# Kernel optimization log

Measured on AMD Instinct MI355X. Metric: run time of the kernel, lower is better.

The kernel has to match this reference:

```python
import jax, jax.numpy as jnp
import numpy as np

N, E, IN, HID, HEADS, OUT = 50000, 800000, 128, 64, 4, 64


def setup_inputs() -> dict:
    key = jax.random.key(0)
    ks = jax.random.split(key, 13)
    s1 = 1.0 / np.sqrt(IN)
    s2 = 1.0 / np.sqrt(HID * HEADS)
    s3 = 1.0 / np.sqrt(HID)
    return {
        'x': jax.random.normal(ks[0], (N, IN), dtype=jnp.float32),
        'edge_index': jax.random.randint(ks[1], (2, E), 0, N, dtype=jnp.int64),
        # GATv2 layer 1: heads=HEADS, out=HID, concat=True
        'W1l': jax.random.normal(ks[2], (IN, HEADS * HID), dtype=jnp.float32) * s1,
        'W1r': jax.random.normal(ks[3], (IN, HEADS * HID), dtype=jnp.float32) * s1,
        'att1': jax.random.normal(ks[4], (HEADS, HID), dtype=jnp.float32) * s3,
        'b1': jnp.zeros((HEADS * HID,), dtype=jnp.float32),
        # GATv2 layer 2: heads=1, out=HID
        'W2l': jax.random.normal(ks[5], (HEADS * HID, HID), dtype=jnp.float32) * s2,
        'W2r': jax.random.normal(ks[6], (HEADS * HID, HID), dtype=jnp.float32) * s2,
        'att2': jax.random.normal(ks[7], (1, HID), dtype=jnp.float32) * s3,
        'b2': jnp.zeros((HID,), dtype=jnp.float32),
        # final Linear(HID, OUT)
        'Wlin': jax.random.normal(ks[8], (HID, OUT), dtype=jnp.float32) * s3,
        'blin': jnp.zeros((OUT,), dtype=jnp.float32),
    }


def _gatv2(x, src, dst, Wl, Wr, att, bias, n):
    # PyG GATv2Conv (share_weights=False): x_j -> lin_l, x_i -> lin_r
    H, C = att.shape
    xl = (x @ Wl).reshape(n, H, C)  # source transform [N,H,C]
    xr = (x @ Wr).reshape(n, H, C)  # destination transform [N,H,C]
    # per-edge GATv2 score: a^T LeakyReLU(xl_j + xr_i)
    e = jnp.sum(jax.nn.leaky_relu(xl[src] + xr[dst], 0.2) * att, axis=-1)  # [E,H]
    # scatter-softmax over edges sharing a destination
    m = jax.ops.segment_max(e, dst, num_segments=n)  # [N,H]
    ex = jnp.exp(e - m[dst])
    denom = jax.ops.segment_sum(ex, dst, num_segments=n)
    alpha = ex / (denom[dst] + 1e-16)  # [E,H]
    # weighted scatter-add aggregation of source features
    out = jax.ops.segment_sum(xl[src] * alpha[:, :, None], dst, num_segments=n)  # [N,H,C]
    return out.reshape(n, H * C) + bias


def reference(x, edge_index, W1l, W1r, att1, b1, W2l, W2r, att2, b2, Wlin, blin):
    n = x.shape[0]
    loops = jnp.arange(n, dtype=edge_index.dtype)
    src = jnp.concatenate([edge_index[0], loops])  # add_self_loops=True (PyG default)
    dst = jnp.concatenate([edge_index[1], loops])
    h = _gatv2(x, src, dst, W1l, W1r, att1, b1, n)
    h = jax.nn.elu(h)
    h = _gatv2(h, src, dst, W2l, W2r, att2, b2, n)
    h = jax.nn.elu(h)
    return h @ Wlin + blin
```

## Files before the change

### kernel.cpp

```cpp
#include <hip/hip_runtime.h>
#include <hip/hip_bf16.h>
#include <math.h>

#define N_NODES 50000
#define N_EDGES 800000
#define ETOT (N_EDGES + N_NODES)
#define NB_SCAN 196

typedef __attribute__((ext_vector_type(8))) short short8;
typedef __attribute__((ext_vector_type(4))) float floatx4;
typedef __attribute__((ext_vector_type(2))) float f32x2;

__device__ __forceinline__ float bf_lo(unsigned u) { return __uint_as_float(u << 16); }
__device__ __forceinline__ float bf_hi(unsigned u) { return __uint_as_float(u & 0xffff0000u); }
__device__ __forceinline__ unsigned short f2bf(float f) {
    unsigned u = __float_as_uint(f);
    return (unsigned short)((u + 0x7fffu + ((u >> 16) & 1u)) >> 16);
}
__device__ __forceinline__ unsigned pack2bf(float a, float b) {
    return (unsigned)f2bf(a) | ((unsigned)f2bf(b) << 16);
}
#define DPP_ADD(p, ctrl) \
    (p) += __int_as_float(__builtin_amdgcn_update_dpp(0, __float_as_int(p), (ctrl), 0xF, 0xF, true))

__global__ __launch_bounds__(256) void k_prep(const float* __restrict__ W1l,
                                              const float* __restrict__ W1r,
                                              const float* __restrict__ W2l,
                                              const float* __restrict__ W2r,
                                              const float* __restrict__ Wlin,
                                              unsigned short* __restrict__ Wt1,
                                              unsigned short* __restrict__ Wt2,
                                              unsigned short* __restrict__ Wt3,
                                              int* __restrict__ deg) {
    const int b = blockIdx.x;
    if (b < 400) {
        const int idx = b * 256 + threadIdx.x;
        if (idx < 65536) {
            const int k = idx >> 9;
            const int n = idx & 511;
            const float v = (n < 256) ? W1l[k * 256 + n] : W1r[k * 256 + (n - 256)];
            Wt1[n * 128 + k] = f2bf(v);
        } else if (idx < 98304) {
            const int j = idx - 65536;
            const int k = j >> 7;
            const int n = j & 127;
            const float v = (n < 64) ? W2l[k * 64 + n] : W2r[k * 64 + (n - 64)];
            Wt2[n * 256 + k] = f2bf(v);
        } else {
            const int j = idx - 98304;
            const int n = j >> 6, k = j & 63;
            Wt3[n * 64 + k] = f2bf(Wlin[k * 64 + n]);
        }
    } else {
        const int i = (b - 400) * 256 + threadIdx.x;
        if (i < N_NODES) deg[i] = 0;
    }
}

__global__ __launch_bounds__(256) void k_g1h(const float* __restrict__ x,
                                             const unsigned short* __restrict__ Wt1,
                                             unsigned short* __restrict__ xlb,
                                             unsigned short* __restrict__ xrb,
                                             const int* __restrict__ ei,
                                             int* __restrict__ deg) {
    __shared__ unsigned short sA[128 * 136];
    const int b = blockIdx.x;
    if (b >= 782) {
        for (long e = (long)(b - 782) * 256 + threadIdx.x; e < ETOT; e += 1024 * 256) {
            const int d = (e < N_EDGES) ? ei[N_EDGES + e] : (int)(e - N_EDGES);
            atomicAdd(&deg[d], 1);
        }
        return;
    }
    const int t = threadIdx.x;
    const int lane = t & 63, wv = t >> 6;
    const int m0 = (b >> 1) * 128;
    const int flavor = b & 1;
#pragma unroll
    for (int j = 0; j < 16; j++) {
        const int i4 = t + j * 256;
        const int row = i4 >> 5, k4 = i4 & 31;
        float4 v = make_float4(0.f, 0.f, 0.f, 0.f);
        if (m0 + row < N_NODES) v = ((const float4*)x)[(long)(m0 + row) * 32 + k4];
        ushort4 u;
        u.x = f2bf(v.x); u.y = f2bf(v.y); u.z = f2bf(v.z); u.w = f2bf(v.w);
        *(ushort4*)&sA[row * 136 + k4 * 4] = u;
    }
    __syncthreads();
    const int l15 = lane & 15, quad = lane >> 4;
    const int nloc0 = wv * 64;
    unsigned short* outp = flavor ? xrb : xlb;
    short8 bfr[4][4];
#pragma unroll
    for (int nt = 0; nt < 4; nt++)
#pragma unroll
        for (int ks = 0; ks < 4; ks++)
            bfr[nt][ks] = *(const short8*)&Wt1[(flavor * 256 + nloc0 + nt * 16 + l15) * 128 + ks * 32 + quad * 8];
    for (int mt = 0; mt < 8; mt++) {
        short8 a[4];
#pragma unroll
        for (int ks = 0; ks < 4; ks++)
            a[ks] = *(const short8*)&sA[(mt * 16 + l15) * 136 + ks * 32 + quad * 8];
        floatx4 acc[4];
#pragma unroll
        for (int nt = 0; nt < 4; nt++) {
            acc[nt] = (floatx4)(0.f);
#pragma unroll
            for (int ks = 0; ks < 4; ks++)
                acc[nt] = __builtin_amdgcn_mfma_f32_16x16x32_bf16(a[ks], bfr[nt][ks], acc[nt], 0, 0, 0);
        }
        const int mrow0 = m0 + mt * 16 + quad * 4;
#pragma unroll
        for (int nt = 0; nt < 4; nt++) {
            const int n = nloc0 + nt * 16 + l15;
#pragma unroll
            for (int r = 0; r < 4; r++) {
                const int m = mrow0 + r;
                if (m < N_NODES) outp[(long)m * 256 + n] = f2bf(acc[nt][r]);
            }
        }
    }
}

__global__ __launch_bounds__(256) void k_scan1(const int* __restrict__ deg,
                                               int* __restrict__ rowstart,
                                               int* __restrict__ blocksum) {
    __shared__ int wsum[4];
    const int t = threadIdx.x, lane = t & 63, wv = t >> 6;
    const int i = blockIdx.x * 256 + t;
    const int v = (i < N_NODES) ? deg[i] : 0;
    int incl = v;
#pragma unroll
    for (int off = 1; off < 64; off <<= 1) {
        const int u = __shfl_up(incl, off);
        if (lane >= off) incl += u;
    }
    if (lane == 63) wsum[wv] = incl;
    __syncthreads();
    int woff = 0;
#pragma unroll
    for (int j = 0; j < 4; j++) woff += (j < wv) ? wsum[j] : 0;
    const int excl = incl - v + woff;
    if (i < N_NODES) rowstart[i] = excl;
    if (t == 255) blocksum[blockIdx.x] = excl + v;
}

__global__ __launch_bounds__(256) void k_scan2(const int* __restrict__ blocksum,
                                               int* __restrict__ blockoff) {
    __shared__ int wsum[4];
    const int t = threadIdx.x, lane = t & 63, wv = t >> 6;
    const int v = (t < NB_SCAN) ? blocksum[t] : 0;
    int incl = v;
#pragma unroll
    for (int off = 1; off < 64; off <<= 1) {
        const int u = __shfl_up(incl, off);
        if (lane >= off) incl += u;
    }
    if (lane == 63) wsum[wv] = incl;
    __syncthreads();
    int woff = 0;
#pragma unroll
    for (int j = 0; j < 4; j++) woff += (j < wv) ? wsum[j] : 0;
    if (t < NB_SCAN) blockoff[t] = incl - v + woff;
}

__global__ __launch_bounds__(256) void k_scan3(int* __restrict__ rowstart,
                                               const int* __restrict__ blockoff,
                                               int* __restrict__ cursor) {
    const int i = blockIdx.x * 256 + threadIdx.x;
    if (i < N_NODES) {
        const int r = rowstart[i] + blockoff[blockIdx.x];
        rowstart[i] = r;
        cursor[i] = r;
    }
}

__global__ __launch_bounds__(256) void k_scatter(const int* __restrict__ ei,
                                                 int* __restrict__ cursor,
                                                 int* __restrict__ csr) {
    const long e = (long)blockIdx.x * 256 + threadIdx.x;
    if (e >= ETOT) return;
    int s, d;
    if (e < N_EDGES) { s = ei[e]; d = ei[N_EDGES + e]; }
    else { s = d = (int)(e - N_EDGES); }
    const int pos = atomicAdd(&cursor[d], 1);
    csr[pos] = s << 9;
}

__global__ __launch_bounds__(256) void k_node1(const int* __restrict__ rowstart,
                                               const int* __restrict__ deg,
                                               const int* __restrict__ csr,
                                               const uint4* __restrict__ xlb,
                                               const uint4* __restrict__ xrb,
                                               const float* __restrict__ att,
                                               const float* __restrict__ b1,
                                               uint4* __restrict__ h1b) {
    const int lane = threadIdx.x & 63;
    const int wv = threadIdx.x >> 6;
    const int node = blockIdx.x * 4 + wv;
    const int g = lane >> 5;
    const int l = lane & 31;
    const char* xlbase = (const char*)xlb;
    const uint4 xru = xrb[(long)node * 32 + l];
    const float4 ta = ((const float4*)att)[2 * l];
    const float4 tb = ((const float4*)att)[2 * l + 1];
    f32x2 xp[4], tp[4];
    xp[0] = (f32x2){bf_lo(xru.x), bf_hi(xru.x)};
    xp[1] = (f32x2){bf_lo(xru.y), bf_hi(xru.y)};
    xp[2] = (f32x2){bf_lo(xru.z), bf_hi(xru.z)};
    xp[3] = (f32x2){bf_lo(xru.w), bf_hi(xru.w)};
    tp[0] = (f32x2){ta.x, ta.y}; tp[1] = (f32x2){ta.z, ta.w};
    tp[2] = (f32x2){tb.x, tb.y}; tp[3] = (f32x2){tb.z, tb.w};
    const int start = rowstart[node];
    const int cnt = deg[node];
    const int ns = (cnt - g + 1) >> 1;
    float den = 0.f;
    f32x2 acc[4];
#pragma unroll
    for (int c = 0; c < 4; c++) acc[c] = (f32x2)(0.f);

    auto body = [&](const uint4& rr) {
        f32x2 a0, a1, a2, a3;
        a0.x = bf_lo(rr.x); a0.y = bf_hi(rr.x);
        a1.x = bf_lo(rr.y); a1.y = bf_hi(rr.y);
        a2.x = bf_lo(rr.z); a2.y = bf_hi(rr.z);
        a3.x = bf_lo(rr.w); a3.y = bf_hi(rr.w);
        f32x2 v = a0 + xp[0];
        f32x2 p2 = __builtin_elementwise_max(v, v * 0.2f) * tp[0];
        v = a1 + xp[1]; p2 += __builtin_elementwise_max(v, v * 0.2f) * tp[1];
        v = a2 + xp[2]; p2 += __builtin_elementwise_max(v, v * 0.2f) * tp[2];
        v = a3 + xp[3]; p2 += __builtin_elementwise_max(v, v * 0.2f) * tp[3];
        float p = p2.x + p2.y;
        DPP_ADD(p, 0xB1);
        DPP_ADD(p, 0x4E);
        DPP_ADD(p, 0x141);
        const float w = __expf(p);
        acc[0] += a0 * w;
        acc[1] += a1 * w;
        acc[2] += a2 * w;
        acc[3] += a3 * w;
        den += w;
    };

    uint4 rcur = make_uint4(0, 0, 0, 0), rnext = rcur;
    if (ns > 0) rcur = *((const uint4*)(xlbase + csr[start + g]) + l);
    if (ns > 1) rnext = *((const uint4*)(xlbase + csr[start + 2 + g]) + l);
    int i = 0;
    for (; i + 2 < ns; i++) {
        const uint4 r2 = *((const uint4*)(xlbase + csr[start + 2 * (i + 2) + g]) + l);
        body(rcur);
        rcur = rnext; rnext = r2;
    }
    for (; i < ns; i++) {
        body(rcur);
        rcur = rnext;
    }
    den += __shfl_xor(den, 32);
    const float inv = 1.f / (den + 1e-16f);
#pragma unroll
    for (int c = 0; c < 4; c++) {
        f32x2 t2 = acc[c];
        t2.x += __shfl_xor(t2.x, 32);
        t2.y += __shfl_xor(t2.y, 32);
        acc[c] = t2;
    }
    const float4 ba = ((const float4*)b1)[2 * l];
    const float4 bb = ((const float4*)b1)[2 * l + 1];
    f32x2 bp[4];
    bp[0] = (f32x2){ba.x, ba.y}; bp[1] = (f32x2){ba.z, ba.w};
    bp[2] = (f32x2){bb.x, bb.y}; bp[3] = (f32x2){bb.z, bb.w};
    float o[8];
#pragma unroll
    for (int c = 0; c < 4; c++) {
        f32x2 t2 = acc[c] * inv + bp[c];
        o[2 * c]     = t2.x > 0.f ? t2.x : expm1f(t2.x);
        o[2 * c + 1] = t2.y > 0.f ? t2.y : expm1f(t2.y);
    }
    if (g == 0) {
        uint4 u;
        u.x = pack2bf(o[0], o[1]);
        u.y = pack2bf(o[2], o[3]);
        u.z = pack2bf(o[4], o[5]);
        u.w = pack2bf(o[6], o[7]);
        h1b[(long)node * 32 + l] = u;
    }
}

__global__ __launch_bounds__(256) void k_gemm2(const uint4* __restrict__ h,
                                               const unsigned short* __restrict__ Wt2,
                                               unsigned short* __restrict__ xlb,
                                               unsigned short* __restrict__ xrb) {
    __shared__ unsigned short sA[64 * 264];
    const int t = threadIdx.x;
    const int lane = t & 63, wv = t >> 6;
    const int m0 = blockIdx.x * 64;
#pragma unroll
    for (int j = 0; j < 8; j++) {
        const int i8 = t + j * 256;
        const int row = i8 >> 5, c8 = i8 & 31;
        uint4 v = make_uint4(0, 0, 0, 0);
        if (m0 + row < N_NODES) v = h[(long)(m0 + row) * 32 + c8];
        *(uint4*)&sA[row * 264 + c8 * 8] = v;
    }
    __syncthreads();
    const int l15 = lane & 15, quad = lane >> 4;
    const int ncol0 = wv * 32;
    short8 b[2][8];
#pragma unroll
    for (int nt = 0; nt < 2; nt++)
#pragma unroll
        for (int ks = 0; ks < 8; ks++)
            b[nt][ks] = *(const short8*)&Wt2[(ncol0 + nt * 16 + l15) * 256 + ks * 32 + quad * 8];
    for (int mt = 0; mt < 4; mt++) {
        floatx4 acc[2];
        acc[0] = (floatx4)(0.f);
        acc[1] = (floatx4)(0.f);
#pragma unroll
        for (int ks = 0; ks < 8; ks++) {
            const short8 a = *(const short8*)&sA[(mt * 16 + l15) * 264 + ks * 32 + quad * 8];
            acc[0] = __builtin_amdgcn_mfma_f32_16x16x32_bf16(a, b[0][ks], acc[0], 0, 0, 0);
            acc[1] = __builtin_amdgcn_mfma_f32_16x16x32_bf16(a, b[1][ks], acc[1], 0, 0, 0);
        }
        const int mrow0 = m0 + mt * 16 + quad * 4;
#pragma unroll
        for (int nt = 0; nt < 2; nt++) {
            const int n = ncol0 + nt * 16 + l15;
#pragma unroll
            for (int r = 0; r < 4; r++) {
                const int m = mrow0 + r;
                if (m < N_NODES) {
                    if (n < 64) xlb[(long)m * 64 + n] = f2bf(acc[nt][r]);
                    else        xrb[(long)m * 64 + (n - 64)] = f2bf(acc[nt][r]);
                }
            }
        }
    }
}

__global__ __launch_bounds__(256) void k_node2(const int* __restrict__ rowstart,
                                               const int* __restrict__ deg,
                                               const int* __restrict__ csr,
                                               const uint2* __restrict__ xlb,
                                               const uint2* __restrict__ xrb,
                                               const float* __restrict__ att,
                                               const float* __restrict__ b2,
                                               uint2* __restrict__ h2b) {
    const int lane = threadIdx.x & 63;
    const int wv = threadIdx.x >> 6;
    const int node = blockIdx.x * 4 + wv;
    const int g = lane >> 4;
    const int l = lane & 15;
    const char* xlbase = (const char*)xlb;
    const uint2 xru = xrb[(long)node * 16 + l];
    const float4 at4 = ((const float4*)att)[l];
    f32x2 xp[2], tp[2];
    xp[0] = (f32x2){bf_lo(xru.x), bf_hi(xru.x)};
    xp[1] = (f32x2){bf_lo(xru.y), bf_hi(xru.y)};
    tp[0] = (f32x2){at4.x, at4.y}; tp[1] = (f32x2){at4.z, at4.w};
    const int start = rowstart[node];
    const int cnt = deg[node];
    const int ns = (cnt - g + 3) >> 2;
    float den = 0.f;
    f32x2 acc[2];
    acc[0] = (f32x2)(0.f); acc[1] = (f32x2)(0.f);

    auto body = [&](const uint2& rr) {
        f32x2 a0, a1;
        a0.x = bf_lo(rr.x); a0.y = bf_hi(rr.x);
        a1.x = bf_lo(rr.y); a1.y = bf_hi(rr.y);
        f32x2 v = a0 + xp[0];
        f32x2 p2 = __builtin_elementwise_max(v, v * 0.2f) * tp[0];
        v = a1 + xp[1]; p2 += __builtin_elementwise_max(v, v * 0.2f) * tp[1];
        float p = p2.x + p2.y;
        DPP_ADD(p, 0xB1);
        DPP_ADD(p, 0x4E);
        DPP_ADD(p, 0x141);
        DPP_ADD(p, 0x140);
        const float w = __expf(p);
        acc[0] += a0 * w;
        acc[1] += a1 * w;
        den += w;
    };

    uint2 rcur = make_uint2(0, 0), rnext = rcur;
    if (ns > 0) rcur = *((const uint2*)(xlbase + (csr[start + g] >> 2)) + l);
    if (ns > 1) rnext = *((const uint2*)(xlbase + (csr[start + 4 + g] >> 2)) + l);
    int i = 0;
    for (; i + 2 < ns; i++) {
        const uint2 r2 = *((const uint2*)(xlbase + (csr[start + 4 * (i + 2) + g] >> 2)) + l);
        body(rcur);
        rcur = rnext; rnext = r2;
    }
    for (; i < ns; i++) {
        body(rcur);
        rcur = rnext;
    }
    den += __shfl_xor(den, 16);
    den += __shfl_xor(den, 32);
    const float inv = 1.f / (den + 1e-16f);
    float t0 = acc[0].x, t1 = acc[0].y, t2 = acc[1].x, t3 = acc[1].y;
    t0 += __shfl_xor(t0, 16); t0 += __shfl_xor(t0, 32);
    t1 += __shfl_xor(t1, 16); t1 += __shfl_xor(t1, 32);
    t2 += __shfl_xor(t2, 16); t2 += __shfl_xor(t2, 32);
    t3 += __shfl_xor(t3, 16); t3 += __shfl_xor(t3, 32);
    const float4 b4 = ((const float4*)b2)[l];
    float4 h4;
    h4.x = t0 * inv + b4.x; h4.x = h4.x > 0.f ? h4.x : expm1f(h4.x);
    h4.y = t1 * inv + b4.y; h4.y = h4.y > 0.f ? h4.y : expm1f(h4.y);
    h4.z = t2 * inv + b4.z; h4.z = h4.z > 0.f ? h4.z : expm1f(h4.z);
    h4.w = t3 * inv + b4.w; h4.w = h4.w > 0.f ? h4.w : expm1f(h4.w);
    if (g == 0) {
        uint2 u;
        u.x = pack2bf(h4.x, h4.y);
        u.y = pack2bf(h4.z, h4.w);
        h2b[(long)node * 16 + l] = u;
    }
}

__global__ __launch_bounds__(256) void k_gemm3(const uint4* __restrict__ h2,
                                               const unsigned short* __restrict__ Wt3,
                                               const float* __restrict__ blin,
                                               float* __restrict__ out) {
    __shared__ unsigned short sA[64 * 72];
    const int t = threadIdx.x;
    const int lane = t & 63, wv = t >> 6;
    const int m0 = blockIdx.x * 64;
#pragma unroll
    for (int j = 0; j < 2; j++) {
        const int i8 = t + j * 256;
        const int row = i8 >> 3, c8 = i8 & 7;
        uint4 v = make_uint4(0, 0, 0, 0);
        if (m0 + row < N_NODES) v = h2[(long)(m0 + row) * 8 + c8];
        *(uint4*)&sA[row * 72 + c8 * 8] = v;
    }
    __syncthreads();
    const int l15 = lane & 15, quad = lane >> 4;
    const int n0 = wv * 16;
    const short8 b0 = *(const short8*)&Wt3[(n0 + l15) * 64 + quad * 8];
    const short8 b1 = *(const short8*)&Wt3[(n0 + l15) * 64 + 32 + quad * 8];
    const float bl = blin[n0 + l15];
#pragma unroll
    for (int mt = 0; mt < 4; mt++) {
        const short8 a0 = *(const short8*)&sA[(mt * 16 + l15) * 72 + quad * 8];
        const short8 a1 = *(const short8*)&sA[(mt * 16 + l15) * 72 + 32 + quad * 8];
        floatx4 acc = (floatx4)(0.f);
        acc = __builtin_amdgcn_mfma_f32_16x16x32_bf16(a0, b0, acc, 0, 0, 0);
        acc = __builtin_amdgcn_mfma_f32_16x16x32_bf16(a1, b1, acc, 0, 0, 0);
        const int mrow0 = m0 + mt * 16 + quad * 4;
#pragma unroll
        for (int r = 0; r < 4; r++) {
            const int m = mrow0 + r;
            if (m < N_NODES) out[(long)m * 64 + n0 + l15] = acc[r] + bl;
        }
    }
}

extern "C" void kernel_launch(void* const* d_in, const int* in_sizes, int n_in,
                              void* d_out, int out_size, void* d_ws, size_t ws_size,
                              hipStream_t stream) {
    (void)in_sizes; (void)n_in; (void)out_size; (void)ws_size;
    const float* x    = (const float*)d_in[0];
    const int*   ei   = (const int*)d_in[1];
    const float* W1l  = (const float*)d_in[2];
    const float* W1r  = (const float*)d_in[3];
    const float* att1 = (const float*)d_in[4];
    const float* b1   = (const float*)d_in[5];
    const float* W2l  = (const float*)d_in[6];
    const float* W2r  = (const float*)d_in[7];
    const float* att2 = (const float*)d_in[8];
    const float* b2   = (const float*)d_in[9];
    const float* Wlin = (const float*)d_in[10];
    const float* blin = (const float*)d_in[11];

    float* ws = (float*)d_ws;
    unsigned short* XL1b = (unsigned short*)(ws);
    uint2*          H2b  = (uint2*)(ws);
    unsigned short* XR1b = (unsigned short*)(ws + 6400000);
    uint4*          H1b  = (uint4*)(ws + 12800000);
    unsigned short* XL2b = (unsigned short*)(ws + 19200000);
    unsigned short* XR2b = (unsigned short*)(ws + 20800000);
    int* deg      = (int*)(ws + 22400000);
    int* rowstart = deg + 50000;
    int* cursor   = rowstart + 50000;
    int* blocksum = cursor + 50000;
    int* blockoff = blocksum + 256;
    int* csr      = blockoff + 256;
    unsigned short* Wt1 = (unsigned short*)(ws + 23500000);
    unsigned short* Wt2 = (unsigned short*)(ws + 23550000);
    unsigned short* Wt3 = (unsigned short*)(ws + 23600000);

    k_prep<<<596, 256, 0, stream>>>(W1l, W1r, W2l, W2r, Wlin, Wt1, Wt2, Wt3, deg);
    k_g1h<<<1806, 256, 0, stream>>>(x, Wt1, XL1b, XR1b, ei, deg);
    k_scan1<<<NB_SCAN, 256, 0, stream>>>(deg, rowstart, blocksum);
    k_scan2<<<1, 256, 0, stream>>>(blocksum, blockoff);
    k_scan3<<<NB_SCAN, 256, 0, stream>>>(rowstart, blockoff, cursor);
    k_scatter<<<(ETOT + 255) / 256, 256, 0, stream>>>(ei, cursor, csr);
    k_node1<<<12500, 256, 0, stream>>>(rowstart, deg, csr,
                                       (const uint4*)XL1b, (const uint4*)XR1b,
                                       att1, b1, H1b);
    k_gemm2<<<782, 256, 0, stream>>>((const uint4*)H1b, Wt2, XL2b, XR2b);
    k_node2<<<12500, 256, 0, stream>>>(rowstart, deg, csr,
                                       (const uint2*)XL2b, (const uint2*)XR2b,
                                       att2, b2, H2b);
    k_gemm3<<<782, 256, 0, stream>>>((const uint4*)H2b, Wt3, blin, (float*)d_out);
}
```

Measured before the change: 309.7 us.

## Merge CSR build into cooperative kernel, widen node1 lanes, use exp2 with prescaled att

Replaces the three scan kernels and the scatter kernel with one cooperative kernel that uses grid-wide syncs, removing three launch boundaries. k_node1 now processes four edges per wave concurrently, with each 16-lane group covering 16 channels (one head), instead of two edges with 32 lanes. Both node kernels switch to a native exp2 with attention vectors prescaled by log2(e) in the prep kernel. This risks cooperative launch limits and adds grid-sync overhead plus higher register pressure in node1.

```diff
diff --git a/kernel.cpp b/kernel.cpp
--- a/kernel.cpp
+++ b/kernel.cpp
@@ -1,6 +1,9 @@
 #include <hip/hip_runtime.h>
 #include <hip/hip_bf16.h>
+#include <hip/hip_cooperative_groups.h>
 #include <math.h>
+
+namespace cg = cooperative_groups;
 
 #define N_NODES 50000
 #define N_EDGES 800000
@@ -23,17 +26,23 @@
 #define DPP_ADD(p, ctrl) \
     (p) += __int_as_float(__builtin_amdgcn_update_dpp(0, __float_as_int(p), (ctrl), 0xF, 0xF, true))
 
+#define LOG2E 1.4426950408889634f
+
 __global__ __launch_bounds__(256) void k_prep(const float* __restrict__ W1l,
                                               const float* __restrict__ W1r,
                                               const float* __restrict__ W2l,
                                               const float* __restrict__ W2r,
                                               const float* __restrict__ Wlin,
+                                              const float* __restrict__ att1,
+                                              const float* __restrict__ att2,
                                               unsigned short* __restrict__ Wt1,
                                               unsigned short* __restrict__ Wt2,
                                               unsigned short* __restrict__ Wt3,
+                                              float* __restrict__ att1s,
+                                              float* __restrict__ att2s,
                                               int* __restrict__ deg) {
     const int b = blockIdx.x;
-    if (b < 400) {
+    if (b < 402) {
         const int idx = b * 256 + threadIdx.x;
         if (idx < 65536) {
             const int k = idx >> 9;
@@ -46,13 +55,19 @@
             const int n = j & 127;
             const float v = (n < 64) ? W2l[k * 64 + n] : W2r[k * 64 + (n - 64)];
             Wt2[n * 256 + k] = f2bf(v);
-        } else {
+        } else if (idx < 102400) {
             const int j = idx - 98304;
             const int n = j >> 6, k = j & 63;
             Wt3[n * 64 + k] = f2bf(Wlin[k * 64 + n]);
+        } else if (idx < 102656) {
+            const int j = idx - 102400;
+            att1s[j] = att1[j] * LOG2E;
+        } else if (idx < 102720) {
+            const int j = idx - 102656;
+            att2s[j] = att2[j] * LOG2E;
         }
     } else {
-        const int i = (b - 400) * 256 + threadIdx.x;
+        const int i = (b - 402) * 256 + threadIdx.x;
         if (i < N_NODES) deg[i] = 0;
     }
 }
@@ -122,167 +137,186 @@
     }
 }
 
-__global__ __launch_bounds__(256) void k_scan1(const int* __restrict__ deg,
-                                               int* __restrict__ rowstart,
-                                               int* __restrict__ blocksum) {
+__global__ __launch_bounds__(256) void k_csr(const int* __restrict__ deg,
+                                             int* __restrict__ rowstart,
+                                             int* __restrict__ blocksum,
+                                             int* __restrict__ blockoff,
+                                             int* __restrict__ cursor,
+                                             const int* __restrict__ ei,
+                                             int* __restrict__ csr) {
+    cg::grid_group grid = cg::this_grid();
     __shared__ int wsum[4];
     const int t = threadIdx.x, lane = t & 63, wv = t >> 6;
-    const int i = blockIdx.x * 256 + t;
-    const int v = (i < N_NODES) ? deg[i] : 0;
-    int incl = v;
-#pragma unroll
-    for (int off = 1; off < 64; off <<= 1) {
-        const int u = __shfl_up(incl, off);
-        if (lane >= off) incl += u;
-    }
-    if (lane == 63) wsum[wv] = incl;
-    __syncthreads();
-    int woff = 0;
-#pragma unroll
-    for (int j = 0; j < 4; j++) woff += (j < wv) ? wsum[j] : 0;
-    const int excl = incl - v + woff;
-    if (i < N_NODES) rowstart[i] = excl;
-    if (t == 255) blocksum[blockIdx.x] = excl + v;
-}
-
-__global__ __launch_bounds__(256) void k_scan2(const int* __restrict__ blocksum,
-                                               int* __restrict__ blockoff) {
-    __shared__ int wsum[4];
-    const int t = threadIdx.x, lane = t & 63, wv = t >> 6;
-    const int v = (t < NB_SCAN) ? blocksum[t] : 0;
-    int incl = v;
-#pragma unroll
-    for (int off = 1; off < 64; off <<= 1) {
-        const int u = __shfl_up(incl, off);
-        if (lane >= off) incl += u;
-    }
-    if (lane == 63) wsum[wv] = incl;
-    __syncthreads();
-    int woff = 0;
-#pragma unroll
-    for (int j = 0; j < 4; j++) woff += (j < wv) ? wsum[j] : 0;
-    if (t < NB_SCAN) blockoff[t] = incl - v + woff;
-}
-
-__global__ __launch_bounds__(256) void k_scan3(int* __restrict__ rowstart,
-                                               const int* __restrict__ blockoff,
-                                               int* __restrict__ cursor) {
-    const int i = blockIdx.x * 256 + threadIdx.x;
-    if (i < N_NODES) {
-        const int r = rowstart[i] + blockoff[blockIdx.x];
-        rowstart[i] = r;
-        cursor[i] = r;
-    }
-}
-
-__global__ __launch_bounds__(256) void k_scatter(const int* __restrict__ ei,
-                                                 int* __restrict__ cursor,
-                                                 int* __restrict__ csr) {
-    const long e = (long)blockIdx.x * 256 + threadIdx.x;
-    if (e >= ETOT) return;
-    int s, d;
-    if (e < N_EDGES) { s = ei[e]; d = ei[N_EDGES + e]; }
-    else { s = d = (int)(e - N_EDGES); }
-    const int pos = atomicAdd(&cursor[d], 1);
-    csr[pos] = s << 9;
-}
-
-__global__ __launch_bounds__(256) void k_node1(const int* __restrict__ rowstart,
-                                               const int* __restrict__ deg,
-                                               const int* __restrict__ csr,
-                                               const uint4* __restrict__ xlb,
-                                               const uint4* __restrict__ xrb,
-                                               const float* __restrict__ att,
-                                               const float* __restrict__ b1,
-                                               uint4* __restrict__ h1b) {
+    if (blockIdx.x < NB_SCAN) {
+        const int i = blockIdx.x * 256 + t;
+        const int v = (i < N_NODES) ? deg[i] : 0;
+        int incl = v;
+#pragma unroll
+        for (int off = 1; off < 64; off <<= 1) {
+            const int u = __shfl_up(incl, off);
+            if (lane >= off) incl += u;
+        }
+        if (lane == 63) wsum[wv] = incl;
+        __syncthreads();
+        int woff = 0;
+#pragma unroll
+        for (int j = 0; j < 4; j++) woff += (j < wv) ? wsum[j] : 0;
+        const int excl = incl - v + woff;
+        if (i < N_NODES) rowstart[i] = excl;
+        if (t == 255) blocksum[blockIdx.x] = excl + v;
+    }
+    grid.sync();
+    if (blockIdx.x == 0) {
+        const int v = (t < NB_SCAN) ? blocksum[t] : 0;
+        int incl = v;
+#pragma unroll
+        for (int off = 1; off < 64; off <<= 1) {
+            const int u = __shfl_up(incl, off);
+            if (lane >= off) incl += u;
+        }
+        __syncthreads();
+        if (lane == 63) wsum[wv] = incl;
+        __syncthreads();
+        int woff = 0;
+#pragma unroll
+        for (int j = 0; j < 4; j++) woff += (j < wv) ? wsum[j] : 0;
+        if (t < NB_SCAN) blockoff[t] = incl - v + woff;
+    }
+    grid.sync();
+    for (int c = blockIdx.x; c < NB_SCAN; c += gridDim.x) {
+        const int i = c * 256 + t;
+        if (i < N_NODES) {
+            const int r = rowstart[i] + blockoff[c];
+            rowstart[i] = r;
+            cursor[i] = r;
+        }
+    }
+    grid.sync();
+    for (long e = (long)blockIdx.x * 256 + t; e < ETOT; e += (long)gridDim.x * 256) {
+        int s, d;
+        if (e < N_EDGES) { s = ei[e]; d = ei[N_EDGES + e]; }
+        else { s = d = (int)(e - N_EDGES); }
+        const int pos = atomicAdd(&cursor[d], 1);
+        csr[pos] = s << 9;
+    }
+}
+
+__global__ __launch_bounds__(256, 4) void k_node1(const int* __restrict__ rowstart,
+                                                  const int* __restrict__ deg,
+                                                  const int* __restrict__ csr,
+                                                  const uint4* __restrict__ xlb,
+                                                  const uint4* __restrict__ xrb,
+                                                  const float* __restrict__ att_s,
+                                                  const float* __restrict__ b1,
+                                                  uint4* __restrict__ h1b) {
     const int lane = threadIdx.x & 63;
     const int wv = threadIdx.x >> 6;
     const int node = blockIdx.x * 4 + wv;
-    const int g = lane >> 5;
-    const int l = lane & 31;
+    const int g = lane >> 4;
+    const int l = lane & 15;
     const char* xlbase = (const char*)xlb;
-    const uint4 xru = xrb[(long)node * 32 + l];
-    const float4 ta = ((const float4*)att)[2 * l];
-    const float4 tb = ((const float4*)att)[2 * l + 1];
-    f32x2 xp[4], tp[4];
-    xp[0] = (f32x2){bf_lo(xru.x), bf_hi(xru.x)};
-    xp[1] = (f32x2){bf_lo(xru.y), bf_hi(xru.y)};
-    xp[2] = (f32x2){bf_lo(xru.z), bf_hi(xru.z)};
-    xp[3] = (f32x2){bf_lo(xru.w), bf_hi(xru.w)};
-    tp[0] = (f32x2){ta.x, ta.y}; tp[1] = (f32x2){ta.z, ta.w};
-    tp[2] = (f32x2){tb.x, tb.y}; tp[3] = (f32x2){tb.z, tb.w};
+    const uint4 xru0 = xrb[(long)node * 32 + 2 * l];
+    const uint4 xru1 = xrb[(long)node * 32 + 2 * l + 1];
+    f32x2 xp[8], tp[8];
+    xp[0] = (f32x2){bf_lo(xru0.x), bf_hi(xru0.x)};
+    xp[1] = (f32x2){bf_lo(xru0.y), bf_hi(xru0.y)};
+    xp[2] = (f32x2){bf_lo(xru0.z), bf_hi(xru0.z)};
+    xp[3] = (f32x2){bf_lo(xru0.w), bf_hi(xru0.w)};
+    xp[4] = (f32x2){bf_lo(xru1.x), bf_hi(xru1.x)};
+    xp[5] = (f32x2){bf_lo(xru1.y), bf_hi(xru1.y)};
+    xp[6] = (f32x2){bf_lo(xru1.z), bf_hi(xru1.z)};
+    xp[7] = (f32x2){bf_lo(xru1.w), bf_hi(xru1.w)};
+    {
+        const float4 ta0 = ((const float4*)att_s)[4 * l];
+        const float4 ta1 = ((const float4*)att_s)[4 * l + 1];
+        const float4 ta2 = ((const float4*)att_s)[4 * l + 2];
+        const float4 ta3 = ((const float4*)att_s)[4 * l + 3];
+        tp[0] = (f32x2){ta0.x, ta0.y}; tp[1] = (f32x2){ta0.z, ta0.w};
+        tp[2] = (f32x2){ta1.x, ta1.y}; tp[3] = (f32x2){ta1.z, ta1.w};
+        tp[4] = (f32x2){ta2.x, ta2.y}; tp[5] = (f32x2){ta2.z, ta2.w};
+        tp[6] = (f32x2){ta3.x, ta3.y}; tp[7] = (f32x2){ta3.z, ta3.w};
+    }
     const int start = rowstart[node];
     const int cnt = deg[node];
-    const int ns = (cnt - g + 1) >> 1;
+    const int ns = (cnt - g + 3) >> 2;
     float den = 0.f;
-    f32x2 acc[4];
-#pragma unroll
-    for (int c = 0; c < 4; c++) acc[c] = (f32x2)(0.f);
-
-    auto body = [&](const uint4& rr) {
-        f32x2 a0, a1, a2, a3;
-        a0.x = bf_lo(rr.x); a0.y = bf_hi(rr.x);
-        a1.x = bf_lo(rr.y); a1.y = bf_hi(rr.y);
-        a2.x = bf_lo(rr.z); a2.y = bf_hi(rr.z);
-        a3.x = bf_lo(rr.w); a3.y = bf_hi(rr.w);
-        f32x2 v = a0 + xp[0];
-        f32x2 p2 = __builtin_elementwise_max(v, v * 0.2f) * tp[0];
-        v = a1 + xp[1]; p2 += __builtin_elementwise_max(v, v * 0.2f) * tp[1];
-        v = a2 + xp[2]; p2 += __builtin_elementwise_max(v, v * 0.2f) * tp[2];
-        v = a3 + xp[3]; p2 += __builtin_elementwise_max(v, v * 0.2f) * tp[3];
+    f32x2 acc[8];
+#pragma unroll
+    for (int c = 0; c < 8; c++) acc[c] = (f32x2)(0.f);
+
+    auto body = [&](const uint4& r0, const uint4& r1) {
+        f32x2 a[8];
+        a[0] = (f32x2){bf_lo(r0.x), bf_hi(r0.x)};
+        a[1] = (f32x2){bf_lo(r0.y), bf_hi(r0.y)};
+        a[2] = (f32x2){bf_lo(r0.z), bf_hi(r0.z)};
+        a[3] = (f32x2){bf_lo(r0.w), bf_hi(r0.w)};
+        a[4] = (f32x2){bf_lo(r1.x), bf_hi(r1.x)};
+        a[5] = (f32x2){bf_lo(r1.y), bf_hi(r1.y)};
+        a[6] = (f32x2){bf_lo(r1.z), bf_hi(r1.z)};
+        a[7] = (f32x2){bf_lo(r1.w), bf_hi(r1.w)};
+        f32x2 p2 = (f32x2)(0.f);
+#pragma unroll
+        for (int c = 0; c < 8; c++) {
+            const f32x2 v = a[c] + xp[c];
+            p2 += __builtin_elementwise_max(v, v * 0.2f) * tp[c];
+        }
         float p = p2.x + p2.y;
         DPP_ADD(p, 0xB1);
         DPP_ADD(p, 0x4E);
-        DPP_ADD(p, 0x141);
-        const float w = __expf(p);
-        acc[0] += a0 * w;
-        acc[1] += a1 * w;
-        acc[2] += a2 * w;
-        acc[3] += a3 * w;
+        const float w = __builtin_amdgcn_exp2f(p);
+#pragma unroll
+        for (int c = 0; c < 8; c++) acc[c] += a[c] * w;
         den += w;
     };
 
-    uint4 rcur = make_uint4(0, 0, 0, 0), rnext = rcur;
-    if (ns > 0) rcur = *((const uint4*)(xlbase + csr[start + g]) + l);
-    if (ns > 1) rnext = *((const uint4*)(xlbase + csr[start + 2 + g]) + l);
+    uint4 c0 = make_uint4(0, 0, 0, 0), c1 = c0, n0 = c0, n1 = c0;
+    if (ns > 0) { const uint4* pb = (const uint4*)(xlbase + csr[start + g]); c0 = pb[2 * l]; c1 = pb[2 * l + 1]; }
+    if (ns > 1) { const uint4* pb = (const uint4*)(xlbase + csr[start + 4 + g]); n0 = pb[2 * l]; n1 = pb[2 * l + 1]; }
     int i = 0;
     for (; i + 2 < ns; i++) {
-        const uint4 r2 = *((const uint4*)(xlbase + csr[start + 2 * (i + 2) + g]) + l);
-        body(rcur);
-        rcur = rnext; rnext = r2;
+        const uint4* pb = (const uint4*)(xlbase + csr[start + 4 * (i + 2) + g]);
+        const uint4 f0 = pb[2 * l], f1 = pb[2 * l + 1];
+        body(c0, c1);
+        c0 = n0; c1 = n1; n0 = f0; n1 = f1;
     }
     for (; i < ns; i++) {
-        body(rcur);
-        rcur = rnext;
-    }
+        body(c0, c1);
+        c0 = n0; c1 = n1;
+    }
+    den += __shfl_xor(den, 16);
     den += __shfl_xor(den, 32);
     const float inv = 1.f / (den + 1e-16f);
 #pragma unroll
-    for (int c = 0; c < 4; c++) {
+    for (int c = 0; c < 8; c++) {
         f32x2 t2 = acc[c];
-        t2.x += __shfl_xor(t2.x, 32);
-        t2.y += __shfl_xor(t2.y, 32);
+        t2.x += __shfl_xor(t2.x, 16); t2.x += __shfl_xor(t2.x, 32);
+        t2.y += __shfl_xor(t2.y, 16); t2.y += __shfl_xor(t2.y, 32);
         acc[c] = t2;
     }
-    const float4 ba = ((const float4*)b1)[2 * l];
-    const float4 bb = ((const float4*)b1)[2 * l + 1];
-    f32x2 bp[4];
-    bp[0] = (f32x2){ba.x, ba.y}; bp[1] = (f32x2){ba.z, ba.w};
-    bp[2] = (f32x2){bb.x, bb.y}; bp[3] = (f32x2){bb.z, bb.w};
-    float o[8];
-#pragma unroll
-    for (int c = 0; c < 4; c++) {
-        f32x2 t2 = acc[c] * inv + bp[c];
-        o[2 * c]     = t2.x > 0.f ? t2.x : expm1f(t2.x);
-        o[2 * c + 1] = t2.y > 0.f ? t2.y : expm1f(t2.y);
-    }
     if (g == 0) {
-        uint4 u;
-        u.x = pack2bf(o[0], o[1]);
-        u.y = pack2bf(o[2], o[3]);
-        u.z = pack2bf(o[4], o[5]);
-        u.w = pack2bf(o[6], o[7]);
-        h1b[(long)node * 32 + l] = u;
+        const float4 bb0 = ((const float4*)b1)[4 * l];
+        const float4 bb1 = ((const float4*)b1)[4 * l + 1];
+        const float4 bb2 = ((const float4*)b1)[4 * l + 2];
+        const float4 bb3 = ((const float4*)b1)[4 * l + 3];
+        f32x2 bp[8];
+        bp[0] = (f32x2){bb0.x, bb0.y}; bp[1] = (f32x2){bb0.z, bb0.w};
+        bp[2] = (f32x2){bb1.x, bb1.y}; bp[3] = (f32x2){bb1.z, bb1.w};
+        bp[4] = (f32x2){bb2.x, bb2.y}; bp[5] = (f32x2){bb2.z, bb2.w};
+        bp[6] = (f32x2){bb3.x, bb3.y}; bp[7] = (f32x2){bb3.z, bb3.w};
+        float o[16];
+#pragma unroll
+        for (int c = 0; c < 8; c++) {
+            const f32x2 t2 = acc[c] * inv + bp[c];
+            o[2 * c]     = t2.x > 0.f ? t2.x : expm1f(t2.x);
+            o[2 * c + 1] = t2.y > 0.f ? t2.y : expm1f(t2.y);
+        }
+        uint4 u0, u1;
+        u0.x = pack2bf(o[0], o[1]);  u0.y = pack2bf(o[2], o[3]);
+        u0.z = pack2bf(o[4], o[5]);  u0.w = pack2bf(o[6], o[7]);
+        u1.x = pack2bf(o[8], o[9]);  u1.y = pack2bf(o[10], o[11]);
+        u1.z = pack2bf(o[12], o[13]); u1.w = pack2bf(o[14], o[15]);
+        h1b[(long)node * 32 + 2 * l] = u0;
+        h1b[(long)node * 32 + 2 * l + 1] = u1;
     }
 }
 
@@ -342,7 +376,7 @@
                                                const int* __restrict__ csr,
                                                const uint2* __restrict__ xlb,
                                                const uint2* __restrict__ xrb,
-                                               const float* __restrict__ att,
+                                               const float* __restrict__ att_s,
                                                const float* __restrict__ b2,
                                                uint2* __restrict__ h2b) {
     const int lane = threadIdx.x & 63;
@@ -352,7 +386,7 @@
     const int l = lane & 15;
     const char* xlbase = (const char*)xlb;
     const uint2 xru = xrb[(long)node * 16 + l];
-    const float4 at4 = ((const float4*)att)[l];
+    const float4 at4 = ((const float4*)att_s)[l];
     f32x2 xp[2], tp[2];
     xp[0] = (f32x2){bf_lo(xru.x), bf_hi(xru.x)};
     xp[1] = (f32x2){bf_lo(xru.y), bf_hi(xru.y)};
@@ -376,7 +410,7 @@
         DPP_ADD(p, 0x4E);
         DPP_ADD(p, 0x141);
         DPP_ADD(p, 0x140);
-        const float w = __expf(p);
+        const float w = __builtin_amdgcn_exp2f(p);
         acc[0] += a0 * w;
         acc[1] += a1 * w;
         den += w;
@@ -488,19 +522,23 @@
     unsigned short* Wt1 = (unsigned short*)(ws + 23500000);
     unsigned short* Wt2 = (unsigned short*)(ws + 23550000);
     unsigned short* Wt3 = (unsigned short*)(ws + 23600000);
-
-    k_prep<<<596, 256, 0, stream>>>(W1l, W1r, W2l, W2r, Wlin, Wt1, Wt2, Wt3, deg);
+    float* att1s = ws + 23610000;
+    float* att2s = ws + 23610256;
+
+    k_prep<<<598, 256, 0, stream>>>(W1l, W1r, W2l, W2r, Wlin, att1, att2,
+                                    Wt1, Wt2, Wt3, att1s, att2s, deg);
     k_g1h<<<1806, 256, 0, stream>>>(x, Wt1, XL1b, XR1b, ei, deg);
-    k_scan1<<<NB_SCAN, 256, 0, stream>>>(deg, rowstart, blocksum);
-    k_scan2<<<1, 256, 0, stream>>>(blocksum, blockoff);
-    k_scan3<<<NB_SCAN, 256, 0, stream>>>(rowstart, blockoff, cursor);
-    k_scatter<<<(ETOT + 255) / 256, 256, 0, stream>>>(ei, cursor, csr);
+    {
+        void* args[] = {(void*)&deg, (void*)&rowstart, (void*)&blocksum,
+                        (void*)&blockoff, (void*)&cursor, (void*)&ei, (void*)&csr};
+        hipLaunchCooperativeKernel((void*)k_csr, dim3(850), dim3(256), args, 0, stream);
+    }
     k_node1<<<12500, 256, 0, stream>>>(rowstart, deg, csr,
                                        (const uint4*)XL1b, (const uint4*)XR1b,
-                                       att1, b1, H1b);
+                                       att1s, b1, H1b);
     k_gemm2<<<782, 256, 0, stream>>>((const uint4*)H1b, Wt2, XL2b, XR2b);
     k_node2<<<12500, 256, 0, stream>>>(rowstart, deg, csr,
                                        (const uint2*)XL2b, (const uint2*)XR2b,
-                                       att2, b2, H2b);
+                                       att2s, b2, H2b);
     k_gemm3<<<782, 256, 0, stream>>>((const uint4*)H2b, Wt3, blin, (float*)d_out);
 }
```

After: 653.2 us. 2.11x slower.
